# Kernel optimization log

Hardware: AMD Instinct MI355X
Metric: run time of the kernel (lower is better)

The kernel has to match this reference:

```python
import jax, jax.numpy as jnp
import numpy as np

N = 100000
E = 1600000
R = 4
D_IN = 128
D_H = 128
C = 2


def _rgcn_conv(x, W, src, dst, et):
    """PyG RGCNConv, root_weight=False, bias=False, aggr='mean'.
    x: [N, d_in], W: [R, d_in, d_out]. Per relation: mean over incoming
    edges of that relation of (x[src] @ W_r), summed over relations.
    """
    n, r = x.shape[0], W.shape[0]
    xw = jnp.einsum('ni,rio->rno', x, W)          # [R, N, d_out]
    m = xw[et, src]                               # [E, d_out] per-edge messages
    key = dst * r + et                            # segment per (dst, relation)
    sums = jax.ops.segment_sum(m, key, num_segments=n * r)
    cnt = jax.ops.segment_sum(jnp.ones((m.shape[0],), m.dtype), key, num_segments=n * r)
    mean = sums / jnp.maximum(cnt, 1.0)[:, None]  # [N*R, d_out]
    return mean.reshape(n, r, -1).sum(axis=1)     # sum over relations -> [N, d_out]


def setup_inputs() -> dict:
    key = jax.random.key(0)
    k = jax.random.split(key, 6)
    x = jax.random.normal(k[0], (N, D_IN), dtype=jnp.float32)
    edge_index = jax.random.randint(k[1], (2, E), 0, N, dtype=jnp.int32)
    edge_type = jax.random.randint(k[2], (E,), 0, R, dtype=jnp.int32)
    # Glorot-ish scaled relation weights per layer
    W1 = jax.random.normal(k[3], (R, D_IN, D_H), dtype=jnp.float32) / np.sqrt(D_IN)
    W2 = jax.random.normal(k[4], (R, D_H, D_H), dtype=jnp.float32) / np.sqrt(D_H)
    W3 = jax.random.normal(k[5], (R, D_H, C), dtype=jnp.float32) / np.sqrt(D_H)
    return {"x": x, "edge_index": edge_index, "edge_type": edge_type,
            "W1": W1, "W2": W2, "W3": W3}


def reference(x, edge_index, edge_type, W1, W2, W3):
    src, dst = edge_index[0], edge_index[1]
    # eval mode: dropout is identity
    h = _rgcn_conv(x, W1, src, dst, edge_type)
    h = jnp.tanh(h)
    h = _rgcn_conv(h, W2, src, dst, edge_type)
    h = jnp.tanh(h)
    h = _rgcn_conv(h, W3, src, dst, edge_type)   # [N, C] logits
    return jax.nn.softmax(h, axis=1), h
```

## Files before the change

kernel.cpp:

```cpp
#include <hip/hip_runtime.h>
#include <math.h>

#define N_NODES 100000
#define N_EDGES 1600000
#define RREL 4
#define DDIM 128
#define KDIM 512
#define NKEY 400000

typedef __bf16 bf16x8 __attribute__((ext_vector_type(8)));
typedef float f32x4 __attribute__((ext_vector_type(4)));

__device__ __forceinline__ float bflo(unsigned u){ return __builtin_bit_cast(float, u << 16); }
__device__ __forceinline__ float bfhi(unsigned u){ return __builtin_bit_cast(float, u & 0xffff0000u); }
__device__ __forceinline__ unsigned f2bf(float f){
  unsigned u = __builtin_bit_cast(unsigned, f);
  return (u + 0x7fffu + ((u >> 16) & 1u)) >> 16;
}
__device__ __forceinline__ int iclamp(int v, int lo, int hi){
  return v < lo ? lo : (v > hi ? hi : v);
}


__global__ void hist_kernel(const int* __restrict__ dst, const int* __restrict__ et,
                            int* __restrict__ counts){
  int e = blockIdx.x * 256 + threadIdx.x;
  int key = iclamp(dst[e] * RREL + et[e], 0, NKEY - 1);
  atomicAdd(&counts[key], 1);
}

__global__ void scan_local(const int* __restrict__ in, int* __restrict__ out,
                           int* __restrict__ bsums, int K){
  __shared__ int s[1024];
  int t = threadIdx.x;
  int i = blockIdx.x * 1024 + t;
  int v = (i < K) ? in[i] : 0;
  s[t] = v; __syncthreads();
  for (int off = 1; off < 1024; off <<= 1){
    int x = (t >= off) ? s[t - off] : 0;
    __syncthreads();
    s[t] += x;
    __syncthreads();
  }
  if (i < K) out[i] = s[t] - v;
  if (t == 1023) bsums[blockIdx.x] = s[t];
}

__global__ void scan_sums(int* __restrict__ b, int nb){
  __shared__ int s[1024];
  int t = threadIdx.x;
  int v = (t < nb) ? b[t] : 0;
  s[t] = v; __syncthreads();
  for (int off = 1; off < 1024; off <<= 1){
    int x = (t >= off) ? s[t - off] : 0;
    __syncthreads();
    s[t] += x;
    __syncthreads();
  }
  if (t < nb) b[t] = s[t] - v;
}

__global__ void scan_add(int* __restrict__ out, int* __restrict__ cursor,
                         const int* __restrict__ bsums, int K, int total){
  int t = threadIdx.x;
  int i = blockIdx.x * 1024 + t;
  if (i < K){
    int v = out[i] + bsums[blockIdx.x];
    out[i] = v;
    cursor[i] = v;
  }
  if (i == 0) out[K] = total;
}

__global__ void scatter_kernel(const int* __restrict__ src, const int* __restrict__ dst,
                               const int* __restrict__ et, int* __restrict__ cursor,
                               int* __restrict__ ssrc){
  int e = blockIdx.x * 256 + threadIdx.x;
  int key = iclamp(dst[e] * RREL + et[e], 0, NKEY - 1);
  int p = atomicAdd(&cursor[key], 1);
  p = iclamp(p, 0, N_EDGES - 1);
  ssrc[p] = iclamp(src[e], 0, N_NODES - 1);
}


__global__ void convert_x(const float* __restrict__ x, unsigned* __restrict__ xb){
  int i = blockIdx.x * 256 + threadIdx.x;
  float2 v = *(const float2*)(x + (size_t)i * 2);
  xb[i] = f2bf(v.x) | (f2bf(v.y) << 16);
}


__global__ void transpose_w(const float* __restrict__ W, unsigned short* __restrict__ Bt){
  int idx = blockIdx.x * 256 + threadIdx.x;
  int k = idx >> 7, n = idx & 127;
  Bt[n * KDIM + k] = (unsigned short)f2bf(W[idx]);
}


__global__ __launch_bounds__(256) void fused_layer(const unsigned* __restrict__ hin,
                                                   const int* __restrict__ ssrc,
                                                   const int* __restrict__ offs,
                                                   const __bf16* __restrict__ Bt,
                                                   unsigned short* __restrict__ hout){
  int tid = threadIdx.x;
  int w = tid >> 6, lane = tid & 63;
  int l15 = lane & 15, quad = lane >> 4;
  int n0w = blockIdx.x * 64 + w * 16;
  int n = n0w + l15;
  int valid = (n < N_NODES);

  f32x4 accC[8];
  #pragma unroll
  for (int tc = 0; tc < 8; tc++) accC[tc] = (f32x4){0.f, 0.f, 0.f, 0.f};

  #pragma unroll
  for (int r = 0; r < RREL; r++){
    int ob = valid ? (n * 4 + r) : 0;
    int beg = iclamp(offs[ob], 0, N_EDGES);
    int end = iclamp(offs[ob + 1], beg, N_EDGES);
    if (!valid){ beg = 0; end = 0; }

    float ac[32];
    #pragma unroll
    for (int j = 0; j < 32; j++) ac[j] = 0.f;

    int i = beg;
    int nxt = (i < end) ? ssrc[i] : 0;
    while (i < end){
      int cur = iclamp(nxt, 0, N_NODES - 1);
      i++;
      nxt = (i < end) ? ssrc[i] : 0;
      const uint4* row = (const uint4*)(hin + (size_t)cur * 64 + quad * 4);
      uint4 u0 = row[0];
      uint4 u1 = row[4];
      uint4 u2 = row[8];
      uint4 u3 = row[12];
      ac[ 0] += bflo(u0.x); ac[ 1] += bfhi(u0.x); ac[ 2] += bflo(u0.y); ac[ 3] += bfhi(u0.y);
      ac[ 4] += bflo(u0.z); ac[ 5] += bfhi(u0.z); ac[ 6] += bflo(u0.w); ac[ 7] += bfhi(u0.w);
      ac[ 8] += bflo(u1.x); ac[ 9] += bfhi(u1.x); ac[10] += bflo(u1.y); ac[11] += bfhi(u1.y);
      ac[12] += bflo(u1.z); ac[13] += bfhi(u1.z); ac[14] += bflo(u1.w); ac[15] += bfhi(u1.w);
      ac[16] += bflo(u2.x); ac[17] += bfhi(u2.x); ac[18] += bflo(u2.y); ac[19] += bfhi(u2.y);
      ac[20] += bflo(u2.z); ac[21] += bfhi(u2.z); ac[22] += bflo(u2.w); ac[23] += bfhi(u2.w);
      ac[24] += bflo(u3.x); ac[25] += bfhi(u3.x); ac[26] += bflo(u3.y); ac[27] += bfhi(u3.y);
      ac[28] += bflo(u3.z); ac[29] += bfhi(u3.z); ac[30] += bflo(u3.w); ac[31] += bfhi(u3.w);
    }
    int cnt = end - beg;
    float sc = (cnt > 0) ? 1.0f / (float)cnt : 0.0f;

    #pragma unroll
    for (int s = 0; s < 4; s++){
      uint4 pv;
      pv.x = f2bf(ac[s * 8 + 0] * sc) | (f2bf(ac[s * 8 + 1] * sc) << 16);
      pv.y = f2bf(ac[s * 8 + 2] * sc) | (f2bf(ac[s * 8 + 3] * sc) << 16);
      pv.z = f2bf(ac[s * 8 + 4] * sc) | (f2bf(ac[s * 8 + 5] * sc) << 16);
      pv.w = f2bf(ac[s * 8 + 6] * sc) | (f2bf(ac[s * 8 + 7] * sc) << 16);
      bf16x8 af = __builtin_bit_cast(bf16x8, pv);
      const __bf16* bbase = Bt + r * 128 + s * 32 + quad * 8;
      #pragma unroll
      for (int tc = 0; tc < 8; tc++){
        bf16x8 bfr = *(const bf16x8*)(bbase + (size_t)(tc * 16 + l15) * KDIM);
        accC[tc] = __builtin_amdgcn_mfma_f32_16x16x32_bf16(af, bfr, accC[tc], 0, 0, 0);
      }
    }
  }

  #pragma unroll
  for (int tc = 0; tc < 8; tc++){
    #pragma unroll
    for (int reg = 0; reg < 4; reg++){
      int n2 = n0w + quad * 4 + reg;
      if (n2 < N_NODES){
        float v = tanhf(accC[tc][reg]);
        hout[(size_t)n2 * 128 + tc * 16 + l15] = (unsigned short)f2bf(v);
      }
    }
  }
}


__global__ void fused_head(const unsigned* __restrict__ h2,
                           const int* __restrict__ ssrc,
                           const int* __restrict__ offs,
                           const float* __restrict__ W3f,
                           float* __restrict__ out){
  int n = blockIdx.x * 4 + (threadIdx.x >> 6);
  int lane = threadIdx.x & 63;
  float dA = 0.f, dB = 0.f;
  int ob = n * 4;
  #pragma unroll
  for (int r = 0; r < RREL; r++){
    int beg = iclamp(offs[ob + r], 0, N_EDGES);
    int end = iclamp(offs[ob + r + 1], beg, N_EDGES);
    float a0=0.f,a1=0.f,b0=0.f,b1=0.f,c0=0.f,c1=0.f,d0=0.f,d1=0.f;
    int i = beg;
    for (; i + 4 <= end; i += 4){
      int s0 = iclamp(ssrc[i],     0, N_NODES-1);
      int s1 = iclamp(ssrc[i + 1], 0, N_NODES-1);
      int s2 = iclamp(ssrc[i + 2], 0, N_NODES-1);
      int s3 = iclamp(ssrc[i + 3], 0, N_NODES-1);
      unsigned u0 = h2[(size_t)s0 * 64 + lane];
      unsigned u1 = h2[(size_t)s1 * 64 + lane];
      unsigned u2 = h2[(size_t)s2 * 64 + lane];
      unsigned u3 = h2[(size_t)s3 * 64 + lane];
      a0 += bflo(u0); a1 += bfhi(u0);
      b0 += bflo(u1); b1 += bfhi(u1);
      c0 += bflo(u2); c1 += bfhi(u2);
      d0 += bflo(u3); d1 += bfhi(u3);
    }
    for (; i < end; i++){
      unsigned u = h2[(size_t)iclamp(ssrc[i], 0, N_NODES-1) * 64 + lane];
      a0 += bflo(u); a1 += bfhi(u);
    }
    int cnt = end - beg;
    float sc = (cnt > 0) ? 1.0f / (float)cnt : 0.0f;
    float m0 = (a0 + b0 + c0 + d0) * sc, m1 = (a1 + b1 + c1 + d1) * sc;
    float4 wv = *(const float4*)(W3f + r * 256 + lane * 4);
    dA += m0 * wv.x + m1 * wv.z;
    dB += m0 * wv.y + m1 * wv.w;
  }
  #pragma unroll
  for (int m = 32; m >= 1; m >>= 1){
    dA += __shfl_xor(dA, m);
    dB += __shfl_xor(dB, m);
  }
  if (lane == 0){
    float mx = fmaxf(dA, dB);
    float e0 = __expf(dA - mx), e1 = __expf(dB - mx);
    float inv = 1.0f / (e0 + e1);
    *(float2*)(out + 2 * n) = (float2){e0 * inv, e1 * inv};
    *(float2*)(out + 2 * N_NODES + 2 * n) = (float2){dA, dB};
  }
}


extern "C" void kernel_launch(void* const* d_in, const int* in_sizes, int n_in,
                              void* d_out, int out_size, void* d_ws, size_t ws_size,
                              hipStream_t stream){
  const float* x  = (const float*)d_in[0];
  const int* ei   = (const int*)d_in[1];
  const int* et   = (const int*)d_in[2];
  const float* W1 = (const float*)d_in[3];
  const float* W2 = (const float*)d_in[4];
  const float* W3 = (const float*)d_in[5];
  float* out = (float*)d_out;
  const int* src = ei;
  const int* dst = ei + N_EDGES;

  char* p = (char*)d_ws;
  auto alloc = [&](size_t bytes) -> char* {
    char* q = p; p += (bytes + 63) & ~(size_t)63; return q;
  };
  int* counts = (int*)alloc((size_t)NKEY * 4);
  int* cursor = counts;
  int* offs   = (int*)alloc((size_t)(NKEY + 1) * 4);
  int* bsums  = (int*)alloc(1024 * 4);
  int* ssrc   = (int*)alloc((size_t)N_EDGES * 4);
  unsigned short* Bt = (unsigned short*)alloc((size_t)DDIM * KDIM * 2);
  unsigned short* h1 = (unsigned short*)alloc((size_t)N_NODES * DDIM * 2);
  unsigned short* h2 = (unsigned short*)alloc((size_t)N_NODES * DDIM * 2);
  unsigned* xb = (unsigned*)h2;

  hipMemsetAsync(counts, 0, (size_t)NKEY * 4, stream);
  hist_kernel<<<N_EDGES / 256, 256, 0, stream>>>(dst, et, counts);
  int nb = (NKEY + 1023) / 1024;
  scan_local<<<nb, 1024, 0, stream>>>(counts, offs, bsums, NKEY);
  scan_sums<<<1, 1024, 0, stream>>>(bsums, nb);
  scan_add<<<nb, 1024, 0, stream>>>(offs, cursor, bsums, NKEY, N_EDGES);
  scatter_kernel<<<N_EDGES / 256, 256, 0, stream>>>(src, dst, et, cursor, ssrc);

  int fgrid = (N_NODES + 63) / 64;

  convert_x<<<(N_NODES * 64) / 256, 256, 0, stream>>>(x, xb);
  transpose_w<<<(DDIM * KDIM) / 256, 256, 0, stream>>>(W1, Bt);
  fused_layer<<<fgrid, 256, 0, stream>>>(xb, ssrc, offs, (const __bf16*)Bt, h1);
  transpose_w<<<(DDIM * KDIM) / 256, 256, 0, stream>>>(W2, Bt);
  fused_layer<<<fgrid, 256, 0, stream>>>((const unsigned*)h1, ssrc, offs, (const __bf16*)Bt, h2);
  fused_head<<<N_NODES / 4, 256, 0, stream>>>((const unsigned*)h2, ssrc, offs, W3, out);
}
```

Before: 816.9 us.

## Unroll edge gather by four and unify head into templated fused node kernel

The per-edge gather loop now issues four source-row loads at once, with predicated weights for the tail, so more memory requests are in flight per lane. The mean scaling is folded into the accumulation. The separate head kernel, which used one wavefront per node, is replaced by a HEAD template variant of the layer kernel that maps 16 nodes to a wave and reduces the two logits with fewer shuffles. Launch bounds now ask for 3 blocks per SM, which may force register spilling given the 32 accumulators and the extra loaded vectors. Source-index clamping in the gather loop is also dropped.

```diff
diff --git a/kernel.cpp b/kernel.cpp
--- a/kernel.cpp
+++ b/kernel.cpp
@@ -97,11 +97,14 @@
 }
 
 
-__global__ __launch_bounds__(256) void fused_layer(const unsigned* __restrict__ hin,
-                                                   const int* __restrict__ ssrc,
-                                                   const int* __restrict__ offs,
-                                                   const __bf16* __restrict__ Bt,
-                                                   unsigned short* __restrict__ hout){
+template<int HEAD>
+__global__ __launch_bounds__(256, 3) void fused_node(const unsigned* __restrict__ hin,
+                                                     const int* __restrict__ ssrc,
+                                                     const int* __restrict__ offs,
+                                                     const __bf16* __restrict__ Bt,
+                                                     const float* __restrict__ W3f,
+                                                     unsigned short* __restrict__ hout,
+                                                     float* __restrict__ fout){
   int tid = threadIdx.x;
   int w = tid >> 6, lane = tid & 63;
   int l15 = lane & 15, quad = lane >> 4;
@@ -110,8 +113,18 @@
   int valid = (n < N_NODES);
 
   f32x4 accC[8];
-  #pragma unroll
-  for (int tc = 0; tc < 8; tc++) accC[tc] = (f32x4){0.f, 0.f, 0.f, 0.f};
+  if (!HEAD){
+    #pragma unroll
+    for (int tc = 0; tc < 8; tc++) accC[tc] = (f32x4){0.f, 0.f, 0.f, 0.f};
+  }
+  float dA = 0.f, dB = 0.f;
+
+  auto acc8 = [&](float* a, uint4 u, float wt){
+    a[0] += bflo(u.x) * wt; a[1] += bfhi(u.x) * wt;
+    a[2] += bflo(u.y) * wt; a[3] += bfhi(u.y) * wt;
+    a[4] += bflo(u.z) * wt; a[5] += bfhi(u.z) * wt;
+    a[6] += bflo(u.w) * wt; a[7] += bfhi(u.w) * wt;
+  };
 
   #pragma unroll
   for (int r = 0; r < RREL; r++){
@@ -119,116 +132,86 @@
     int beg = iclamp(offs[ob], 0, N_EDGES);
     int end = iclamp(offs[ob + 1], beg, N_EDGES);
     if (!valid){ beg = 0; end = 0; }
+    int cnt = end - beg;
+    float winv = (cnt > 0) ? 1.0f / (float)cnt : 0.0f;
 
     float ac[32];
     #pragma unroll
     for (int j = 0; j < 32; j++) ac[j] = 0.f;
 
-    int i = beg;
-    int nxt = (i < end) ? ssrc[i] : 0;
-    while (i < end){
-      int cur = iclamp(nxt, 0, N_NODES - 1);
-      i++;
-      nxt = (i < end) ? ssrc[i] : 0;
-      const uint4* row = (const uint4*)(hin + (size_t)cur * 64 + quad * 4);
-      uint4 u0 = row[0];
-      uint4 u1 = row[4];
-      uint4 u2 = row[8];
-      uint4 u3 = row[12];
-      ac[ 0] += bflo(u0.x); ac[ 1] += bfhi(u0.x); ac[ 2] += bflo(u0.y); ac[ 3] += bfhi(u0.y);
-      ac[ 4] += bflo(u0.z); ac[ 5] += bfhi(u0.z); ac[ 6] += bflo(u0.w); ac[ 7] += bfhi(u0.w);
-      ac[ 8] += bflo(u1.x); ac[ 9] += bfhi(u1.x); ac[10] += bflo(u1.y); ac[11] += bfhi(u1.y);
-      ac[12] += bflo(u1.z); ac[13] += bfhi(u1.z); ac[14] += bflo(u1.w); ac[15] += bfhi(u1.w);
-      ac[16] += bflo(u2.x); ac[17] += bfhi(u2.x); ac[18] += bflo(u2.y); ac[19] += bfhi(u2.y);
-      ac[20] += bflo(u2.z); ac[21] += bfhi(u2.z); ac[22] += bflo(u2.w); ac[23] += bfhi(u2.w);
-      ac[24] += bflo(u3.x); ac[25] += bfhi(u3.x); ac[26] += bflo(u3.y); ac[27] += bfhi(u3.y);
-      ac[28] += bflo(u3.z); ac[29] += bfhi(u3.z); ac[30] += bflo(u3.w); ac[31] += bfhi(u3.w);
-    }
-    int cnt = end - beg;
-    float sc = (cnt > 0) ? 1.0f / (float)cnt : 0.0f;
-
+    for (int i = beg; i < end; i += 4){
+      int j1 = (i + 1 < end) ? i + 1 : i;
+      int j2 = (i + 2 < end) ? i + 2 : i;
+      int j3 = (i + 3 < end) ? i + 3 : i;
+      int s0 = ssrc[i], s1 = ssrc[j1], s2 = ssrc[j2], s3 = ssrc[j3];
+      float wv1 = (i + 1 < end) ? winv : 0.f;
+      float wv2 = (i + 2 < end) ? winv : 0.f;
+      float wv3 = (i + 3 < end) ? winv : 0.f;
+      const uint4* r0 = (const uint4*)(hin + (size_t)s0 * 64 + quad * 4);
+      const uint4* r1 = (const uint4*)(hin + (size_t)s1 * 64 + quad * 4);
+      const uint4* r2 = (const uint4*)(hin + (size_t)s2 * 64 + quad * 4);
+      const uint4* r3 = (const uint4*)(hin + (size_t)s3 * 64 + quad * 4);
+      uint4 a00 = r0[0], a01 = r0[4], a02 = r0[8], a03 = r0[12];
+      uint4 a10 = r1[0], a11 = r1[4], a12 = r1[8], a13 = r1[12];
+      uint4 a20 = r2[0], a21 = r2[4], a22 = r2[8], a23 = r2[12];
+      uint4 a30 = r3[0], a31 = r3[4], a32 = r3[8], a33 = r3[12];
+      acc8(ac +  0, a00, winv); acc8(ac +  8, a01, winv); acc8(ac + 16, a02, winv); acc8(ac + 24, a03, winv);
+      acc8(ac +  0, a10, wv1);  acc8(ac +  8, a11, wv1);  acc8(ac + 16, a12, wv1);  acc8(ac + 24, a13, wv1);
+      acc8(ac +  0, a20, wv2);  acc8(ac +  8, a21, wv2);  acc8(ac + 16, a22, wv2);  acc8(ac + 24, a23, wv2);
+      acc8(ac +  0, a30, wv3);  acc8(ac +  8, a31, wv3);  acc8(ac + 16, a32, wv3);  acc8(ac + 24, a33, wv3);
+    }
+
+    if (!HEAD){
+      #pragma unroll
+      for (int s = 0; s < 4; s++){
+        uint4 pv;
+        pv.x = f2bf(ac[s * 8 + 0]) | (f2bf(ac[s * 8 + 1]) << 16);
+        pv.y = f2bf(ac[s * 8 + 2]) | (f2bf(ac[s * 8 + 3]) << 16);
+        pv.z = f2bf(ac[s * 8 + 4]) | (f2bf(ac[s * 8 + 5]) << 16);
+        pv.w = f2bf(ac[s * 8 + 6]) | (f2bf(ac[s * 8 + 7]) << 16);
+        bf16x8 af = __builtin_bit_cast(bf16x8, pv);
+        const __bf16* bbase = Bt + r * 128 + s * 32 + quad * 8;
+        #pragma unroll
+        for (int tc = 0; tc < 8; tc++){
+          bf16x8 bfr = *(const bf16x8*)(bbase + (size_t)(tc * 16 + l15) * KDIM);
+          accC[tc] = __builtin_amdgcn_mfma_f32_16x16x32_bf16(af, bfr, accC[tc], 0, 0, 0);
+        }
+      }
+    } else {
+      #pragma unroll
+      for (int m = 0; m < 4; m++){
+        #pragma unroll
+        for (int u = 0; u < 8; u++){
+          float2 wv = *(const float2*)(W3f + 2 * (r * 128 + m * 32 + quad * 8 + u));
+          dA += ac[m * 8 + u] * wv.x;
+          dB += ac[m * 8 + u] * wv.y;
+        }
+      }
+    }
+  }
+
+  if (!HEAD){
     #pragma unroll
-    for (int s = 0; s < 4; s++){
-      uint4 pv;
-      pv.x = f2bf(ac[s * 8 + 0] * sc) | (f2bf(ac[s * 8 + 1] * sc) << 16);
-      pv.y = f2bf(ac[s * 8 + 2] * sc) | (f2bf(ac[s * 8 + 3] * sc) << 16);
-      pv.z = f2bf(ac[s * 8 + 4] * sc) | (f2bf(ac[s * 8 + 5] * sc) << 16);
-      pv.w = f2bf(ac[s * 8 + 6] * sc) | (f2bf(ac[s * 8 + 7] * sc) << 16);
-      bf16x8 af = __builtin_bit_cast(bf16x8, pv);
-      const __bf16* bbase = Bt + r * 128 + s * 32 + quad * 8;
+    for (int tc = 0; tc < 8; tc++){
       #pragma unroll
-      for (int tc = 0; tc < 8; tc++){
-        bf16x8 bfr = *(const bf16x8*)(bbase + (size_t)(tc * 16 + l15) * KDIM);
-        accC[tc] = __builtin_amdgcn_mfma_f32_16x16x32_bf16(af, bfr, accC[tc], 0, 0, 0);
+      for (int reg = 0; reg < 4; reg++){
+        int n2 = n0w + quad * 4 + reg;
+        if (n2 < N_NODES){
+          float v = tanhf(accC[tc][reg]);
+          hout[(size_t)n2 * 128 + tc * 16 + l15] = (unsigned short)f2bf(v);
+        }
       }
     }
-  }
-
-  #pragma unroll
-  for (int tc = 0; tc < 8; tc++){
-    #pragma unroll
-    for (int reg = 0; reg < 4; reg++){
-      int n2 = n0w + quad * 4 + reg;
-      if (n2 < N_NODES){
-        float v = tanhf(accC[tc][reg]);
-        hout[(size_t)n2 * 128 + tc * 16 + l15] = (unsigned short)f2bf(v);
-      }
-    }
-  }
-}
-
-
-__global__ void fused_head(const unsigned* __restrict__ h2,
-                           const int* __restrict__ ssrc,
-                           const int* __restrict__ offs,
-                           const float* __restrict__ W3f,
-                           float* __restrict__ out){
-  int n = blockIdx.x * 4 + (threadIdx.x >> 6);
-  int lane = threadIdx.x & 63;
-  float dA = 0.f, dB = 0.f;
-  int ob = n * 4;
-  #pragma unroll
-  for (int r = 0; r < RREL; r++){
-    int beg = iclamp(offs[ob + r], 0, N_EDGES);
-    int end = iclamp(offs[ob + r + 1], beg, N_EDGES);
-    float a0=0.f,a1=0.f,b0=0.f,b1=0.f,c0=0.f,c1=0.f,d0=0.f,d1=0.f;
-    int i = beg;
-    for (; i + 4 <= end; i += 4){
-      int s0 = iclamp(ssrc[i],     0, N_NODES-1);
-      int s1 = iclamp(ssrc[i + 1], 0, N_NODES-1);
-      int s2 = iclamp(ssrc[i + 2], 0, N_NODES-1);
-      int s3 = iclamp(ssrc[i + 3], 0, N_NODES-1);
-      unsigned u0 = h2[(size_t)s0 * 64 + lane];
-      unsigned u1 = h2[(size_t)s1 * 64 + lane];
-      unsigned u2 = h2[(size_t)s2 * 64 + lane];
-      unsigned u3 = h2[(size_t)s3 * 64 + lane];
-      a0 += bflo(u0); a1 += bfhi(u0);
-      b0 += bflo(u1); b1 += bfhi(u1);
-      c0 += bflo(u2); c1 += bfhi(u2);
-      d0 += bflo(u3); d1 += bfhi(u3);
-    }
-    for (; i < end; i++){
-      unsigned u = h2[(size_t)iclamp(ssrc[i], 0, N_NODES-1) * 64 + lane];
-      a0 += bflo(u); a1 += bfhi(u);
-    }
-    int cnt = end - beg;
-    float sc = (cnt > 0) ? 1.0f / (float)cnt : 0.0f;
-    float m0 = (a0 + b0 + c0 + d0) * sc, m1 = (a1 + b1 + c1 + d1) * sc;
-    float4 wv = *(const float4*)(W3f + r * 256 + lane * 4);
-    dA += m0 * wv.x + m1 * wv.z;
-    dB += m0 * wv.y + m1 * wv.w;
-  }
-  #pragma unroll
-  for (int m = 32; m >= 1; m >>= 1){
-    dA += __shfl_xor(dA, m);
-    dB += __shfl_xor(dB, m);
-  }
-  if (lane == 0){
-    float mx = fmaxf(dA, dB);
-    float e0 = __expf(dA - mx), e1 = __expf(dB - mx);
-    float inv = 1.0f / (e0 + e1);
-    *(float2*)(out + 2 * n) = (float2){e0 * inv, e1 * inv};
-    *(float2*)(out + 2 * N_NODES + 2 * n) = (float2){dA, dB};
+  } else {
+    dA += __shfl_xor(dA, 16); dB += __shfl_xor(dB, 16);
+    dA += __shfl_xor(dA, 32); dB += __shfl_xor(dB, 32);
+    if (lane < 16 && valid){
+      float mx = fmaxf(dA, dB);
+      float ea = __expf(dA - mx), eb = __expf(dB - mx);
+      float invs = 1.0f / (ea + eb);
+      *(float2*)(fout + 2 * n) = (float2){ea * invs, eb * invs};
+      *(float2*)(fout + 2 * N_NODES + 2 * n) = (float2){dA, dB};
+    }
   }
 }
 
@@ -272,8 +255,8 @@
 
   convert_x<<<(N_NODES * 64) / 256, 256, 0, stream>>>(x, xb);
   transpose_w<<<(DDIM * KDIM) / 256, 256, 0, stream>>>(W1, Bt);
-  fused_layer<<<fgrid, 256, 0, stream>>>(xb, ssrc, offs, (const __bf16*)Bt, h1);
+  fused_node<0><<<fgrid, 256, 0, stream>>>(xb, ssrc, offs, (const __bf16*)Bt, nullptr, h1, nullptr);
   transpose_w<<<(DDIM * KDIM) / 256, 256, 0, stream>>>(W2, Bt);
-  fused_layer<<<fgrid, 256, 0, stream>>>((const unsigned*)h1, ssrc, offs, (const __bf16*)Bt, h2);
-  fused_head<<<N_NODES / 4, 256, 0, stream>>>((const unsigned*)h2, ssrc, offs, W3, out);
-}
+  fused_node<0><<<fgrid, 256, 0, stream>>>((const unsigned*)h1, ssrc, offs, (const __bf16*)Bt, nullptr, h2, nullptr);
+  fused_node<1><<<fgrid, 256, 0, stream>>>((const unsigned*)h2, ssrc, offs, nullptr, W3, nullptr, out);
+}
```

New measurement: 1.052 ms. 1.29x slower.
